# Optimization experiments

Measured on AMD Instinct MI355X. Metric: run time of the kernel, lower is better.

Reference implementation:

```python
import jax, jax.numpy as jnp
import numpy as np

N_NODES = 50000
N_EDGES = 800000
HIDDEN = 64
HEADS = 8
ADIM = 8
CLAMP = 5.0


def _sqrt_relu(x):
    # sqrt(relu(x)) with backward-safe formulation (identical forward values)
    pos = x > 0
    return jnp.where(pos, jnp.sqrt(jnp.where(pos, x, 1.0)), 0.0)


def _scatter_softmax(score, dst, num_nodes):
    # pyg_softmax: group-wise stable softmax over edges grouped by dst
    m = jax.ops.segment_max(score, dst, num_segments=num_nodes)
    e = jnp.exp(score - m[dst])
    s = jax.ops.segment_sum(e, dst, num_segments=num_nodes)
    return e / (s[dst] + 1e-16)


def setup_inputs() -> dict:
    key = jax.random.key(0)
    ks = jax.random.split(key, 8)
    hd = HEADS * ADIM
    x = jax.random.normal(ks[0], (N_NODES, HIDDEN), dtype=jnp.float32)
    conn_feat = jax.random.normal(ks[1], (N_EDGES, HIDDEN), dtype=jnp.float32)
    edge_index = jax.random.randint(ks[2], (2, N_EDGES), 0, N_NODES)
    qkv_weight = jax.random.normal(ks[3], (3 * hd, HIDDEN), dtype=jnp.float32) * 0.1
    qkv_bias = jnp.zeros((3 * hd,), dtype=jnp.float32)
    E_weight = jax.random.normal(ks[4], (2 * hd, HIDDEN), dtype=jnp.float32) * 0.1
    E_bias = jnp.zeros((2 * hd,), dtype=jnp.float32)
    Aw = jax.random.normal(ks[5], (ADIM, HEADS, 1), dtype=jnp.float32) * 0.3
    Bw = jax.random.normal(ks[6], (ADIM, HEADS, ADIM), dtype=jnp.float32) * 0.3
    return {"x": x, "conn_feat": conn_feat, "edge_index": edge_index,
            "qkv_weight": qkv_weight, "qkv_bias": qkv_bias,
            "E_weight": E_weight, "E_bias": E_bias, "Aw": Aw, "Bw": Bw}


def reference(x, conn_feat, edge_index, qkv_weight, qkv_bias, E_weight, E_bias, Aw, Bw):
    N = x.shape[0]
    hd = HEADS * ADIM
    # packed QKV projection
    qkv = x @ qkv_weight.T + qkv_bias            # [N, 3*hd]
    Qh, Kh, Vh = jnp.split(qkv, 3, axis=-1)      # each [N, hd]
    # edge feature projection -> Ew, Eb
    Eh = (conn_feat @ E_weight.T + E_bias).reshape(-1, 2, hd)
    Ew, Eb = Eh[:, 0, :], Eh[:, 1, :]            # [E, hd]
    dst, src = edge_index[0], edge_index[1]
    # gather-compute: signed-sqrt fused score chain
    conn1 = (Qh[dst] + Kh[src]) * Ew             # [E, hd]
    conn2 = _sqrt_relu(conn1) - _sqrt_relu(-conn1)
    conn = jax.nn.relu(conn2 + Eb)               # act = relu; Eo output
    connh = conn.reshape(-1, HEADS, ADIM)        # [E, h, d]
    score = jnp.einsum('ehd,dhc->ehc', connh, Aw)  # [E, h, 1]
    score = jnp.clip(score, -CLAMP, CLAMP)
    score = _scatter_softmax(score, dst, N)
    # attn_drop_prob = 0 -> dropout is identity
    Vsrc = Vh[src].reshape(-1, HEADS, ADIM)
    agg = jax.ops.segment_sum(Vsrc * score, dst, num_segments=N)    # [N, h, d]
    rowV = jax.ops.segment_sum(connh * score, dst, num_segments=N)  # [N, h, d]
    rowV = jnp.einsum('nhd,dhc->nhc', rowV, Bw)
    No = (agg + rowV).reshape(N, hd)
    return No, conn
```

## Files before the change

kernel.cpp:

```cpp
#include <hip/hip_runtime.h>
#include <cstdint>
#include <cmath>

#define N_NODESC 50000
#define N_EDGESC 800000


__global__ __launch_bounds__(256) void k_zero(int* __restrict__ p, int n) {
  int i = blockIdx.x * 256 + threadIdx.x;
  if (i < n) p[i] = 0;
}

__global__ __launch_bounds__(256) void k_qkv(
    const float* __restrict__ x, const float* __restrict__ w,
    const float* __restrict__ bias, float* __restrict__ qkv, int N)
{
  __shared__ float wT[32 * 193];
  __shared__ float xT[32 * 65];
  const int tid = threadIdx.x;
  const int node0 = blockIdx.x * 64;
  const int tn = tid & 15;
  const int tj = tid >> 4;

  float acc[4][12];
#pragma unroll
  for (int i = 0; i < 4; ++i)
#pragma unroll
    for (int p = 0; p < 12; ++p) acc[i][p] = 0.f;

  for (int kh = 0; kh < 2; ++kh) {
#pragma unroll
    for (int it = 0; it < 6; ++it) {
      int idx4 = tid + it * 256;
      int j = idx4 >> 3;
      int k4 = idx4 & 7;
      float4 a = *(const float4*)&w[j * 64 + kh * 32 + k4 * 4];
      wT[(k4 * 4 + 0) * 193 + j] = a.x;
      wT[(k4 * 4 + 1) * 193 + j] = a.y;
      wT[(k4 * 4 + 2) * 193 + j] = a.z;
      wT[(k4 * 4 + 3) * 193 + j] = a.w;
    }
#pragma unroll
    for (int it = 0; it < 2; ++it) {
      int idx4 = tid + it * 256;
      int n = idx4 >> 3;
      int k4 = idx4 & 7;
      int gn = node0 + n;
      float4 a = make_float4(0.f, 0.f, 0.f, 0.f);
      if (gn < N) a = *(const float4*)&x[gn * 64 + kh * 32 + k4 * 4];
      xT[(k4 * 4 + 0) * 65 + n] = a.x;
      xT[(k4 * 4 + 1) * 65 + n] = a.y;
      xT[(k4 * 4 + 2) * 65 + n] = a.z;
      xT[(k4 * 4 + 3) * 65 + n] = a.w;
    }
    __syncthreads();
#pragma unroll 8
    for (int k = 0; k < 32; ++k) {
      float xa[4], wa[12];
#pragma unroll
      for (int i = 0; i < 4; ++i) xa[i] = xT[k * 65 + tn * 4 + i];
#pragma unroll
      for (int p = 0; p < 12; ++p) wa[p] = wT[k * 193 + tj * 12 + p];
#pragma unroll
      for (int i = 0; i < 4; ++i)
#pragma unroll
        for (int p = 0; p < 12; ++p)
          acc[i][p] = fmaf(xa[i], wa[p], acc[i][p]);
    }
    __syncthreads();
  }

  float b[12];
#pragma unroll
  for (int p = 0; p < 12; ++p) b[p] = bias[tj * 12 + p];
#pragma unroll
  for (int i = 0; i < 4; ++i) {
    int gn = node0 + tn * 4 + i;
    if (gn < N) {
      float* o = &qkv[gn * 192 + tj * 12];
#pragma unroll
      for (int p = 0; p < 12; ++p) o[p] = acc[i][p] + b[p];
    }
  }
}

__global__ __launch_bounds__(256) void k_edge(
    const float* __restrict__ cf, const int* __restrict__ ei,
    const float* __restrict__ ew, const float* __restrict__ ebias,
    const float* __restrict__ qkv, float* __restrict__ conn_out,
    int* __restrict__ counts, int E)
{
  __shared__ float aT[64 * 128];
  __shared__ float bT[64 * 128];
  const int tid = threadIdx.x;
  const int e0 = blockIdx.x * 128;
  const int te = tid >> 4;
  const int tj = tid & 15;

#pragma unroll
  for (int it = 0; it < 8; ++it) {
    int idx = tid + it * 256;
    int j = idx >> 4;
    int k4 = idx & 15;
    float4 a = *(const float4*)&ew[j * 64 + k4 * 4];
    int js = (((j >> 2) ^ k4) << 2) | (j & 3);
    bT[(k4 * 4 + 0) * 128 + js] = a.x;
    bT[(k4 * 4 + 1) * 128 + js] = a.y;
    bT[(k4 * 4 + 2) * 128 + js] = a.z;
    bT[(k4 * 4 + 3) * 128 + js] = a.w;
  }
#pragma unroll
  for (int it = 0; it < 8; ++it) {
    int idx = tid + it * 256;
    int e = idx >> 4;
    int k4 = idx & 15;
    float4 a = *(const float4*)&cf[(e0 + e) * 64 + k4 * 4];
    int es = (((e >> 2) ^ k4) << 2) | (e & 3);
    aT[(k4 * 4 + 0) * 128 + es] = a.x;
    aT[(k4 * 4 + 1) * 128 + es] = a.y;
    aT[(k4 * 4 + 2) * 128 + es] = a.z;
    aT[(k4 * 4 + 3) * 128 + es] = a.w;
  }
  __syncthreads();

  float acc[2][4][8];
#pragma unroll
  for (int g = 0; g < 2; ++g)
#pragma unroll
    for (int i = 0; i < 4; ++i)
#pragma unroll
      for (int c = 0; c < 8; ++c) acc[g][i][c] = 0.f;

#pragma unroll 2
  for (int k4 = 0; k4 < 16; ++k4) {
    const int sA0 = ((te ^ k4) << 2);
    const int sB0 = ((tj ^ k4) << 2);
#pragma unroll
    for (int c = 0; c < 4; ++c) {
      const int k = k4 * 4 + c;
      float4 a0 = *(const float4*)&aT[k * 128 + sA0];
      float4 a1 = *(const float4*)&aT[k * 128 + sA0 + 64];
      float4 b0 = *(const float4*)&bT[k * 128 + sB0];
      float4 b1 = *(const float4*)&bT[k * 128 + sB0 + 64];
      const float av0[4] = {a0.x, a0.y, a0.z, a0.w};
      const float av1[4] = {a1.x, a1.y, a1.z, a1.w};
      const float bv0[4] = {b0.x, b0.y, b0.z, b0.w};
      const float bv1[4] = {b1.x, b1.y, b1.z, b1.w};
#pragma unroll
      for (int i = 0; i < 4; ++i)
#pragma unroll
        for (int j = 0; j < 4; ++j) {
          acc[0][i][j]     = fmaf(av0[i], bv0[j], acc[0][i][j]);
          acc[0][i][4 + j] = fmaf(av0[i], bv1[j], acc[0][i][4 + j]);
          acc[1][i][j]     = fmaf(av1[i], bv0[j], acc[1][i][j]);
          acc[1][i][4 + j] = fmaf(av1[i], bv1[j], acc[1][i][4 + j]);
        }
    }
  }

  float bE[4], bB[4];
#pragma unroll
  for (int c = 0; c < 4; ++c) {
    bE[c] = ebias[tj * 4 + c];
    bB[c] = ebias[64 + tj * 4 + c];
  }
#pragma unroll
  for (int g = 0; g < 2; ++g)
#pragma unroll
    for (int i = 0; i < 4; ++i) {
      const int el = g * 64 + te * 4 + i;
      const int e = e0 + el;
      const int dst = ei[e];
      const int src = ei[E + e];
      float4 q  = *(const float4*)&qkv[dst * 192 + tj * 4];
      float4 kk = *(const float4*)&qkv[src * 192 + 64 + tj * 4];
      const float qv[4] = {q.x, q.y, q.z, q.w};
      const float kv[4] = {kk.x, kk.y, kk.z, kk.w};
      float4 out;
      float ov[4];
#pragma unroll
      for (int c = 0; c < 4; ++c) {
        float aE = acc[g][i][c] + bE[c];
        float aB = acc[g][i][4 + c] + bB[c];
        float s = (qv[c] + kv[c]) * aE;
        float r = sqrtf(fabsf(s));
        float c2 = (s >= 0.f) ? r : -r;
        ov[c] = fmaxf(c2 + aB, 0.f);
      }
      out.x = ov[0]; out.y = ov[1]; out.z = ov[2]; out.w = ov[3];
      *(float4*)&conn_out[(size_t)e * 64 + tj * 4] = out;
      if (tj == 0) atomicAdd(&counts[dst], 1);
    }
}

__global__ void k_scan(const int* __restrict__ counts, int* __restrict__ offsets,
                       int* __restrict__ cursor, int n)
{
  __shared__ int sh[1024];
  const int tid = threadIdx.x;
  const int per = (n + 1023) >> 10;
  int start = tid * per;
  int end = start + per; if (end > n) end = n;
  int sum = 0;
  for (int i = start; i < end && start < n; ++i) sum += counts[i];
  sh[tid] = sum;
  __syncthreads();
  for (int off = 1; off < 1024; off <<= 1) {
    int t = (tid >= off) ? sh[tid - off] : 0;
    __syncthreads();
    if (tid >= off) sh[tid] += t;
    __syncthreads();
  }
  int incl = sh[tid];
  int run = incl - sum;
  for (int i = start; i < end && start < n; ++i) {
    offsets[i] = run; cursor[i] = run; run += counts[i];
  }
  if (tid == 1023) offsets[n] = incl;
}

__global__ __launch_bounds__(256) void k_scatter(const int* __restrict__ ei,
    int* __restrict__ cursor, int* __restrict__ perm, int E)
{
  int e = blockIdx.x * 256 + threadIdx.x;
  if (e < E) {
    int dst = ei[e];
    int pos = atomicAdd(&cursor[dst], 1);
    perm[pos] = e;
  }
}

__global__ __launch_bounds__(256) void k_node(
    const int* __restrict__ ei, const int* __restrict__ offsets,
    const int* __restrict__ perm, const float* __restrict__ conn,
    const float* __restrict__ qkv, const float* __restrict__ Aw,
    const float* __restrict__ Bw, float* __restrict__ No, int N, int E)
{
  const int lane = threadIdx.x & 63;
  int node = blockIdx.x * 4 + (threadIdx.x >> 6);
  node = __builtin_amdgcn_readfirstlane(node);
  if (node >= N) return;

  const float awv = Aw[(lane & 7) * 8 + (lane >> 3)];
  float bw[8];
#pragma unroll
  for (int dd = 0; dd < 8; ++dd) bw[dd] = Bw[dd * 64 + lane];

  const int beg = offsets[node];
  const int end = offsets[node + 1];
  float m = -INFINITY, l = 0.f, aV = 0.f, aC = 0.f;

  float c_nxt = 0.f, v_nxt = 0.f;
  if (beg < end) {
    int e = perm[beg];
    int src = ei[E + e];
    c_nxt = conn[(size_t)e * 64 + lane];
    v_nxt = qkv[src * 192 + 128 + lane];
  }
  for (int i = beg; i < end; ++i) {
    float c = c_nxt;
    float v = v_nxt;
    if (i + 1 < end) {
      int e2 = perm[i + 1];
      int s2 = ei[E + e2];
      c_nxt = conn[(size_t)e2 * 64 + lane];
      v_nxt = qkv[s2 * 192 + 128 + lane];
    }
    float t = c * awv;
    t += __shfl_xor(t, 1, 64);
    t += __shfl_xor(t, 2, 64);
    t += __shfl_xor(t, 4, 64);
    float s = fminf(fmaxf(t, -5.f), 5.f);
    float mn = fmaxf(m, s);
    float al = __expf(m - mn);
    float wgt = __expf(s - mn);
    l  = l * al + wgt;
    aV = fmaf(wgt, v, aV * al);
    aC = fmaf(wgt, c, aC * al);
    m = mn;
  }

  float inv = 1.f / (l + 1e-16f);
  float rowv = aC * inv;
  float acc = aV * inv;
  const int hbase = lane & 56;
#pragma unroll
  for (int dd = 0; dd < 8; ++dd) {
    float rr = __shfl(rowv, hbase + dd, 64);
    acc = fmaf(rr, bw[dd], acc);
  }
  No[node * 64 + lane] = acc;
}

extern "C" void kernel_launch(void* const* d_in, const int* in_sizes, int n_in,
                              void* d_out, int out_size, void* d_ws, size_t ws_size,
                              hipStream_t stream)
{
  const float* x  = (const float*)d_in[0];
  const float* cf = (const float*)d_in[1];
  const int*   ei = (const int*)d_in[2];
  const float* qw = (const float*)d_in[3];
  const float* qb = (const float*)d_in[4];
  const float* ew = (const float*)d_in[5];
  const float* eb = (const float*)d_in[6];
  const float* Aw = (const float*)d_in[7];
  const float* Bw = (const float*)d_in[8];

  float* No   = (float*)d_out;
  float* conn = (float*)d_out + (size_t)N_NODESC * 64;

  char* ws = (char*)d_ws;
  float* QKV   = (float*)(ws);
  int* counts  = (int*)(ws + 38400000);
  int* offsets = (int*)(ws + 38600000);
  int* cursor  = (int*)(ws + 38800004);
  int* perm    = (int*)(ws + 39000004);

  k_zero<<<(N_NODESC + 255) / 256, 256, 0, stream>>>(counts, N_NODESC);
  k_qkv<<<(N_NODESC + 63) / 64, 256, 0, stream>>>(x, qw, qb, QKV, N_NODESC);
  k_edge<<<N_EDGESC / 128, 256, 0, stream>>>(cf, ei, ew, eb, QKV, conn, counts, N_EDGESC);
  k_scan<<<1, 1024, 0, stream>>>(counts, offsets, cursor, N_NODESC);
  k_scatter<<<(N_EDGESC + 255) / 256, 256, 0, stream>>>(ei, cursor, perm, N_EDGESC);
  k_node<<<N_NODESC / 4, 256, 0, stream>>>(ei, offsets, perm, conn, QKV, Aw, Bw, No, N_NODESC, N_EDGESC);
}
```

Baseline: 833.9 us.

## Compute edge projection with split-bf16 MFMA instead of FP32 FMA

The edge-feature projection GEMM moves from scalar FP32 FMAs with transposed shared-memory tiles to MFMA 16x16x32 bf16 instructions. Each operand is split into a high and a low bf16 part and three MFMAs are summed, which keeps accuracy close to FP32. A new prep kernel converts and swizzles the E weight into a bf16 hi/lo buffer in the workspace once per call. The epilogue now does scalar per-lane gathers and stores in the MFMA output layout. The weight buffer shares workspace space with the cursor array, which is only safe because of the launch order.

```diff
diff --git a/kernel.cpp b/kernel.cpp
--- a/kernel.cpp
+++ b/kernel.cpp
@@ -5,10 +5,35 @@
 #define N_NODESC 50000
 #define N_EDGESC 800000
 
+typedef __bf16 bf16x8 __attribute__((ext_vector_type(8)));
+typedef float  f32x4  __attribute__((ext_vector_type(4)));
+
 
 __global__ __launch_bounds__(256) void k_zero(int* __restrict__ p, int n) {
   int i = blockIdx.x * 256 + threadIdx.x;
   if (i < n) p[i] = 0;
+}
+
+__global__ __launch_bounds__(256) void k_prep(const float* __restrict__ ew,
+                                              char* __restrict__ out)
+{
+  int idx = blockIdx.x * 256 + threadIdx.x;
+  int j = idx >> 3;
+  int c = idx & 7;
+  float4 a = *(const float4*)&ew[j * 64 + c * 8];
+  float4 b = *(const float4*)&ew[j * 64 + c * 8 + 4];
+  float f[8] = {a.x, a.y, a.z, a.w, b.x, b.y, b.z, b.w};
+  bf16x8 hv, lv;
+#pragma unroll
+  for (int i = 0; i < 8; ++i) {
+    float fv = f[i];
+    __bf16 h = (__bf16)fv;
+    hv[i] = h;
+    lv[i] = (__bf16)(fv - (float)h);
+  }
+  int swz = c ^ (j & 7);
+  *(bf16x8*)(out + j * 128 + swz * 16) = hv;
+  *(bf16x8*)(out + 16384 + j * 128 + swz * 16) = lv;
 }
 
 __global__ __launch_bounds__(256) void k_qkv(
@@ -86,111 +111,109 @@
 
 __global__ __launch_bounds__(256) void k_edge(
     const float* __restrict__ cf, const int* __restrict__ ei,
-    const float* __restrict__ ew, const float* __restrict__ ebias,
+    const float* __restrict__ ebias, const char* __restrict__ ewb,
     const float* __restrict__ qkv, float* __restrict__ conn_out,
     int* __restrict__ counts, int E)
 {
-  __shared__ float aT[64 * 128];
-  __shared__ float bT[64 * 128];
-  const int tid = threadIdx.x;
-  const int e0 = blockIdx.x * 128;
-  const int te = tid >> 4;
-  const int tj = tid & 15;
-
-#pragma unroll
-  for (int it = 0; it < 8; ++it) {
-    int idx = tid + it * 256;
-    int j = idx >> 4;
-    int k4 = idx & 15;
-    float4 a = *(const float4*)&ew[j * 64 + k4 * 4];
-    int js = (((j >> 2) ^ k4) << 2) | (j & 3);
-    bT[(k4 * 4 + 0) * 128 + js] = a.x;
-    bT[(k4 * 4 + 1) * 128 + js] = a.y;
-    bT[(k4 * 4 + 2) * 128 + js] = a.z;
-    bT[(k4 * 4 + 3) * 128 + js] = a.w;
-  }
-#pragma unroll
-  for (int it = 0; it < 8; ++it) {
-    int idx = tid + it * 256;
-    int e = idx >> 4;
-    int k4 = idx & 15;
-    float4 a = *(const float4*)&cf[(e0 + e) * 64 + k4 * 4];
-    int es = (((e >> 2) ^ k4) << 2) | (e & 3);
-    aT[(k4 * 4 + 0) * 128 + es] = a.x;
-    aT[(k4 * 4 + 1) * 128 + es] = a.y;
-    aT[(k4 * 4 + 2) * 128 + es] = a.z;
-    aT[(k4 * 4 + 3) * 128 + es] = a.w;
-  }
+  __shared__ uint4 Bsh4[2048];
+  char* Bsh = (char*)Bsh4;
+  const int tid  = threadIdx.x;
+  const int lane = tid & 63;
+  const int lr   = lane & 15;
+  const int lg   = lane >> 4;
+  const int wave = tid >> 6;
+  const int e0   = blockIdx.x * 128 + wave * 32;
+
+  uint4 breg[8];
+#pragma unroll
+  for (int it = 0; it < 8; ++it)
+    breg[it] = *(const uint4*)(ewb + tid * 16 + it * 4096);
+
+  float af[2][2][8];
+#pragma unroll
+  for (int t = 0; t < 2; ++t)
+#pragma unroll
+    for (int s = 0; s < 2; ++s) {
+      const float* p = &cf[(size_t)(e0 + t * 16 + lr) * 64 + s * 32 + lg * 8];
+      float4 x0 = *(const float4*)p;
+      float4 x1 = *(const float4*)(p + 4);
+      af[t][s][0] = x0.x; af[t][s][1] = x0.y; af[t][s][2] = x0.z; af[t][s][3] = x0.w;
+      af[t][s][4] = x1.x; af[t][s][5] = x1.y; af[t][s][6] = x1.z; af[t][s][7] = x1.w;
+    }
+
+#pragma unroll
+  for (int it = 0; it < 8; ++it)
+    *(uint4*)(Bsh + tid * 16 + it * 4096) = breg[it];
+
+  bf16x8 ah[2][2], al[2][2];
+#pragma unroll
+  for (int t = 0; t < 2; ++t)
+#pragma unroll
+    for (int s = 0; s < 2; ++s)
+#pragma unroll
+      for (int i = 0; i < 8; ++i) {
+        float fv = af[t][s][i];
+        __bf16 h = (__bf16)fv;
+        ah[t][s][i] = h;
+        al[t][s][i] = (__bf16)(fv - (float)h);
+      }
+
   __syncthreads();
 
-  float acc[2][4][8];
-#pragma unroll
-  for (int g = 0; g < 2; ++g)
-#pragma unroll
-    for (int i = 0; i < 4; ++i)
-#pragma unroll
-      for (int c = 0; c < 8; ++c) acc[g][i][c] = 0.f;
-
-#pragma unroll 2
-  for (int k4 = 0; k4 < 16; ++k4) {
-    const int sA0 = ((te ^ k4) << 2);
-    const int sB0 = ((tj ^ k4) << 2);
-#pragma unroll
-    for (int c = 0; c < 4; ++c) {
-      const int k = k4 * 4 + c;
-      float4 a0 = *(const float4*)&aT[k * 128 + sA0];
-      float4 a1 = *(const float4*)&aT[k * 128 + sA0 + 64];
-      float4 b0 = *(const float4*)&bT[k * 128 + sB0];
-      float4 b1 = *(const float4*)&bT[k * 128 + sB0 + 64];
-      const float av0[4] = {a0.x, a0.y, a0.z, a0.w};
-      const float av1[4] = {a1.x, a1.y, a1.z, a1.w};
-      const float bv0[4] = {b0.x, b0.y, b0.z, b0.w};
-      const float bv1[4] = {b1.x, b1.y, b1.z, b1.w};
-#pragma unroll
-      for (int i = 0; i < 4; ++i)
-#pragma unroll
-        for (int j = 0; j < 4; ++j) {
-          acc[0][i][j]     = fmaf(av0[i], bv0[j], acc[0][i][j]);
-          acc[0][i][4 + j] = fmaf(av0[i], bv1[j], acc[0][i][4 + j]);
-          acc[1][i][j]     = fmaf(av1[i], bv0[j], acc[1][i][j]);
-          acc[1][i][4 + j] = fmaf(av1[i], bv1[j], acc[1][i][4 + j]);
-        }
-    }
-  }
-
-  float bE[4], bB[4];
-#pragma unroll
-  for (int c = 0; c < 4; ++c) {
-    bE[c] = ebias[tj * 4 + c];
-    bB[c] = ebias[64 + tj * 4 + c];
-  }
-#pragma unroll
-  for (int g = 0; g < 2; ++g)
-#pragma unroll
-    for (int i = 0; i < 4; ++i) {
-      const int el = g * 64 + te * 4 + i;
-      const int e = e0 + el;
+  f32x4 acc[2][8];
+#pragma unroll
+  for (int t = 0; t < 2; ++t)
+#pragma unroll
+    for (int ct = 0; ct < 8; ++ct)
+      acc[t][ct] = (f32x4){0.f, 0.f, 0.f, 0.f};
+
+#pragma unroll
+  for (int s = 0; s < 2; ++s) {
+    const int swz = ((s * 4 + lg) ^ (lr & 7)) * 16;
+#pragma unroll
+    for (int ct = 0; ct < 8; ++ct) {
+      const int j = ct * 16 + lr;
+      const bf16x8 bh = *(const bf16x8*)(Bsh + j * 128 + swz);
+      const bf16x8 bl = *(const bf16x8*)(Bsh + 16384 + j * 128 + swz);
+#pragma unroll
+      for (int t = 0; t < 2; ++t) {
+        acc[t][ct] = __builtin_amdgcn_mfma_f32_16x16x32_bf16(ah[t][s], bh, acc[t][ct], 0, 0, 0);
+        acc[t][ct] = __builtin_amdgcn_mfma_f32_16x16x32_bf16(al[t][s], bh, acc[t][ct], 0, 0, 0);
+        acc[t][ct] = __builtin_amdgcn_mfma_f32_16x16x32_bf16(ah[t][s], bl, acc[t][ct], 0, 0, 0);
+      }
+    }
+  }
+
+  float be[4], bb[4];
+#pragma unroll
+  for (int ct = 0; ct < 4; ++ct) {
+    be[ct] = ebias[ct * 16 + lr];
+    bb[ct] = ebias[64 + ct * 16 + lr];
+  }
+
+#pragma unroll
+  for (int t = 0; t < 2; ++t) {
+#pragma unroll
+    for (int r = 0; r < 4; ++r) {
+      const int e   = e0 + t * 16 + lg * 4 + r;
       const int dst = ei[e];
       const int src = ei[E + e];
-      float4 q  = *(const float4*)&qkv[dst * 192 + tj * 4];
-      float4 kk = *(const float4*)&qkv[src * 192 + 64 + tj * 4];
-      const float qv[4] = {q.x, q.y, q.z, q.w};
-      const float kv[4] = {kk.x, kk.y, kk.z, kk.w};
-      float4 out;
-      float ov[4];
-#pragma unroll
-      for (int c = 0; c < 4; ++c) {
-        float aE = acc[g][i][c] + bE[c];
-        float aB = acc[g][i][4 + c] + bB[c];
-        float s = (qv[c] + kv[c]) * aE;
-        float r = sqrtf(fabsf(s));
-        float c2 = (s >= 0.f) ? r : -r;
-        ov[c] = fmaxf(c2 + aB, 0.f);
+      const float* qrow = &qkv[(size_t)dst * 192];
+      const float* krow = &qkv[(size_t)src * 192 + 64];
+      float* orow = &conn_out[(size_t)e * 64];
+#pragma unroll
+      for (int ct = 0; ct < 4; ++ct) {
+        const int j = ct * 16 + lr;
+        float aE = acc[t][ct][r]     + be[ct];
+        float aB = acc[t][ct + 4][r] + bb[ct];
+        float sv = (qrow[j] + krow[j]) * aE;
+        float rt = sqrtf(fabsf(sv));
+        float c2 = (sv >= 0.f) ? rt : -rt;
+        orow[j] = fmaxf(c2 + aB, 0.f);
       }
-      out.x = ov[0]; out.y = ov[1]; out.z = ov[2]; out.w = ov[3];
-      *(float4*)&conn_out[(size_t)e * 64 + tj * 4] = out;
-      if (tj == 0) atomicAdd(&counts[dst], 1);
-    }
+      if (lr == 0) atomicAdd(&counts[dst], 1);
+    }
+  }
 }
 
 __global__ void k_scan(const int* __restrict__ counts, int* __restrict__ offsets,
@@ -314,11 +337,13 @@
   int* counts  = (int*)(ws + 38400000);
   int* offsets = (int*)(ws + 38600000);
   int* cursor  = (int*)(ws + 38800004);
+  char* ewb    = ws + 38800016;
   int* perm    = (int*)(ws + 39000004);
 
   k_zero<<<(N_NODESC + 255) / 256, 256, 0, stream>>>(counts, N_NODESC);
+  k_prep<<<4, 256, 0, stream>>>(ew, ewb);
   k_qkv<<<(N_NODESC + 63) / 64, 256, 0, stream>>>(x, qw, qb, QKV, N_NODESC);
-  k_edge<<<N_EDGESC / 128, 256, 0, stream>>>(cf, ei, ew, eb, QKV, conn, counts, N_EDGESC);
+  k_edge<<<N_EDGESC / 128, 256, 0, stream>>>(cf, ei, eb, ewb, QKV, conn, counts, N_EDGESC);
   k_scan<<<1, 1024, 0, stream>>>(counts, offsets, cursor, N_NODESC);
   k_scatter<<<(N_EDGESC + 255) / 256, 256, 0, stream>>>(ei, cursor, perm, N_EDGESC);
   k_node<<<N_NODESC / 4, 256, 0, stream>>>(ei, offsets, perm, conn, QKV, Aw, Bw, No, N_NODESC, N_EDGESC);
```

New measurement: 765.1 us. -8.3%, faster.
